# Kernel tuning notes

Measured on AMD Instinct MI355X. Metric: run time of the kernel, lower is better.

The kernel has to match this reference:

```python
import jax, jax.numpy as jnp
import numpy as np

B, L, H, P = 4, 8192, 256, 256


def discretize(log_real, imag, log_Delta, B_real, B_imag):
    # Lambda = -exp(log_real) + i*imag ; ZOH discretization
    Lr = -jnp.exp(log_real)
    Li = imag
    Delta = jnp.exp(log_Delta)
    ad = Lr * Delta
    bd = Li * Delta
    exp_ad = jnp.exp(ad)
    Lbar_r = exp_ad * jnp.cos(bd)
    Lbar_i = exp_ad * jnp.sin(bd)
    denom = jnp.maximum(Lr * Lr + Li * Li, 1e-12)
    inv_Lr = Lr / denom
    inv_Li = -Li / denom
    diff_r = Lbar_r - 1.0
    diff_i = Lbar_i
    coeff_r = inv_Lr * diff_r - inv_Li * diff_i
    coeff_i = inv_Lr * diff_i + inv_Li * diff_r
    B_bar_r = coeff_r[:, None] * B_real - coeff_i[:, None] * B_imag
    B_bar_i = coeff_r[:, None] * B_imag + coeff_i[:, None] * B_real
    return Lbar_r, Lbar_i, B_bar_r, B_bar_i


def binop(ei, ej):
    Ar_i, Ai_i, xr_i, xi_i = ei
    Ar_j, Ai_j, xr_j, xi_j = ej
    return (Ar_j * Ar_i - Ai_j * Ai_i,
            Ar_j * Ai_i + Ai_j * Ar_i,
            Ar_j * xr_i - Ai_j * xi_i + xr_j,
            Ar_j * xi_i + Ai_j * xr_i + xi_j)


def apply_ssm(Lbar_r, Lbar_i, B_bar_r, B_bar_i, C_real, C_imag, D, x):
    # x: (B,L,H), B_bar: (P,H), C: (H,P)
    Bu_r = jnp.einsum('blh,ph->blp', x, B_bar_r)
    Bu_i = jnp.einsum('blh,ph->blp', x, B_bar_i)
    A_r = jnp.broadcast_to(Lbar_r, Bu_r.shape)
    A_i = jnp.broadcast_to(Lbar_i, Bu_i.shape)
    _, _, xs_r, xs_i = jax.lax.associative_scan(binop, (A_r, A_i, Bu_r, Bu_i), axis=1)
    ys = jnp.einsum('blp,hp->blh', xs_r, C_real) - jnp.einsum('blp,hp->blh', xs_i, C_imag)
    return ys + D * x


def s5(log_real, imag, log_Delta, B_real, B_imag, C_real, C_imag, D, x):
    Lbar_r, Lbar_i, B_bar_r, B_bar_i = discretize(log_real, imag, log_Delta, B_real, B_imag)
    y = apply_ssm(Lbar_r, Lbar_i, B_bar_r, B_bar_i, C_real, C_imag, D, x)
    return jax.nn.gelu(y, approximate=False)


def setup_inputs() -> dict:
    key = jax.random.key(0)
    ks = jax.random.split(key, 17)
    std_b = 1.0 / H ** 0.5
    std_c = 1.0 / P ** 0.5
    def params(ki):
        k = jax.random.split(ks[ki], 8)
        return dict(
            log_real=jax.random.normal(k[0], (P,), jnp.float32) * 0.5,
            imag=jax.random.normal(k[1], (P,), jnp.float32),
            log_Delta=jnp.zeros((P,), jnp.float32),
            B_real=jax.random.normal(k[2], (P, H), jnp.float32) * std_b,
            B_imag=jax.random.normal(k[3], (P, H), jnp.float32) * std_b,
            C_real=jax.random.normal(k[4], (H, P), jnp.float32) * std_c,
            C_imag=jax.random.normal(k[5], (H, P), jnp.float32) * std_c,
            D=jnp.ones((H,), jnp.float32),
        )
    f = params(1)
    b = params(2)
    inp = {'x': jax.random.normal(ks[0], (B, L, H), jnp.float32)}
    for name, v in f.items():
        inp['fwd_' + name] = v
    for name, v in b.items():
        inp['bwd_' + name] = v
    return inp


def reference(x,
              fwd_log_real, fwd_imag, fwd_log_Delta, fwd_B_real, fwd_B_imag,
              fwd_C_real, fwd_C_imag, fwd_D,
              bwd_log_real, bwd_imag, bwd_log_Delta, bwd_B_real, bwd_B_imag,
              bwd_C_real, bwd_C_imag, bwd_D):
    x_flip = jnp.flip(x, axis=1)
    y_f = s5(fwd_log_real, fwd_imag, fwd_log_Delta, fwd_B_real, fwd_B_imag,
             fwd_C_real, fwd_C_imag, fwd_D, x)
    y_b = s5(bwd_log_real, bwd_imag, bwd_log_Delta, bwd_B_real, bwd_B_imag,
             bwd_C_real, bwd_C_imag, bwd_D, x_flip)
    return y_f + jnp.flip(y_b, axis=1)
```

## Files before the change

### kernel.cpp

```cpp
#include <hip/hip_runtime.h>
#include <math.h>

#define B_DIM 4
#define L_DIM 8192
#define H_DIM 256
#define P_DIM 256
#define M_DIM (B_DIM * L_DIM)
#define NC 64
#define LC 128

typedef __attribute__((ext_vector_type(8))) short bf16x8;
typedef __attribute__((ext_vector_type(4))) float f32x4;

static __device__ __forceinline__ float bf2f(unsigned int u) {
    union { unsigned int i; float f; } v; v.i = u << 16; return v.f;
}
static __device__ __forceinline__ unsigned short f2bf(float f) {
    union { float f; unsigned int i; } v; v.f = f;
    unsigned int r = v.i + 0x7FFFu + ((v.i >> 16) & 1u);
    return (unsigned short)(r >> 16);
}
static __device__ __forceinline__ float gelu_f(float x) {
    float z = 0.7978845608028654f * (x + 0.044715f * x * x * x);
    float e = __expf(2.0f * z);
    float t = 1.0f - 2.0f / (e + 1.0f);
    return 0.5f * x * (1.0f + t);
}
static __device__ __forceinline__ void async_load16(const void* g, void* l) {
    __builtin_amdgcn_global_load_lds(
        (const __attribute__((address_space(1))) unsigned int*)g,
        (__attribute__((address_space(3))) unsigned int*)l, 16, 0, 0);
}
static __device__ __forceinline__ float2 cmul2(float2 a, float2 b) {
    return make_float2(a.x * b.x - a.y * b.y, a.x * b.y + a.y * b.x);
}
static __device__ __forceinline__ float2 csq2(float2 a) {
    return make_float2(a.x * a.x - a.y * a.y, 2.f * a.x * a.y);
}
static __device__ __forceinline__ float2 cmad(float2 A, float2 s, float2 z) {
    return make_float2(A.x * s.x - A.y * s.y + z.x, A.x * s.y + A.y * s.x + z.y);
}

__global__ void prep_kernel(const float* fLr, const float* fIm, const float* fLd,
                            const float* fBr, const float* fBi,
                            const float* fCr, const float* fCi,
                            const float* bLr, const float* bIm, const float* bLd,
                            const float* bBr, const float* bBi,
                            const float* bCr, const float* bCi,
                            const float4* __restrict__ x4, ushort4* __restrict__ xb,
                            unsigned short* Bmat, unsigned short* B3, float2* LbarWS) {
    int gid = blockIdx.x * 256 + threadIdx.x;
    if (gid < 2097152) {
        float4 v = x4[gid];
        ushort4 o;
        o.x = f2bf(v.x); o.y = f2bf(v.y); o.z = f2bf(v.z); o.w = f2bf(v.w);
        xb[gid] = o;
        return;
    }
    int g1 = gid - 2097152;
    if (g1 < 262144) {
        int k = g1 >> 8, h = g1 & 255;
        int d = k >> 9, pc = k & 511, p = pc >> 1, comp = pc & 1;
        const float* LR = d ? bLr : fLr;
        const float* IM = d ? bIm : fIm;
        const float* LD = d ? bLd : fLd;
        const float* BR = d ? bBr : fBr;
        const float* BI = d ? bBi : fBi;
        float Lr = -expf(LR[p]);
        float Li = IM[p];
        float Delta = expf(LD[p]);
        float ea = expf(Lr * Delta);
        float bd = Li * Delta;
        float Lbr = ea * cosf(bd);
        float Lbi = ea * sinf(bd);
        float denom = fmaxf(Lr * Lr + Li * Li, 1e-12f);
        float ivr = Lr / denom, ivi = -Li / denom;
        float dr = Lbr - 1.0f, di = Lbi;
        float cr = ivr * dr - ivi * di;
        float ci = ivr * di + ivi * dr;
        float br = BR[p * 256 + h], bi = BI[p * 256 + h];
        float val = comp ? (cr * bi + ci * br) : (cr * br - ci * bi);
        Bmat[g1] = f2bf(val);
    } else if (g1 < 524288) {
        int g2 = g1 - 262144;
        int d = g2 >> 17;
        int rem = g2 & 131071;
        int h = rem >> 9;
        int kk = rem & 511;
        int p = kk >> 1, comp = kk & 1;
        const float* CR = d ? bCr : fCr;
        const float* CI = d ? bCi : fCi;
        float val = comp ? -CI[h * 256 + p] : CR[h * 256 + p];
        B3[g2] = f2bf(val);
    } else if (g1 < 524800) {
        int g2 = g1 - 524288;
        int d = g2 >> 8, p = g2 & 255;
        const float* LR = d ? bLr : fLr;
        const float* IM = d ? bIm : fIm;
        const float* LD = d ? bLd : fLd;
        float Lr = -expf(LR[p]); float Li = IM[p]; float Delta = expf(LD[p]);
        float ea = expf(Lr * Delta); float bd = Li * Delta;
        LbarWS[g2] = make_float2(ea * cosf(bd), ea * sinf(bd));
    }
}

__global__ __launch_bounds__(256, 2) void k1_gemm(const unsigned short* __restrict__ A,
                                                  const unsigned short* __restrict__ Bm,
                                                  unsigned short* __restrict__ Bu,
                                                  const float2* __restrict__ Lbar,
                                                  float2* __restrict__ carry,
                                                  float2* __restrict__ Usub) {
    __shared__ unsigned short SH[16384];
    __shared__ float2 Sbuf2[64][4];
    int tid = threadIdx.x;
    int lane = tid & 63, wv = tid >> 6;
    int wm = (wv >> 1) * 64, wn = (wv & 1) * 64;
    int Mb = blockIdx.x * 128, Nb = blockIdx.y * 128;
    int lr = lane >> 3;
    int swz = ((lane & 7) ^ lr) * 8;
    f32x4 acc[4][4];
#pragma unroll
    for (int i = 0; i < 4; i++)
#pragma unroll
        for (int j = 0; j < 4; j++) acc[i][j] = (f32x4){0.f, 0.f, 0.f, 0.f};
    int mrow = lane & 15, quad = lane >> 4;
    for (int kb = 0; kb < 256; kb += 64) {
#pragma unroll
        for (int ch = wv; ch < 16; ch += 4) {
            int r = ch * 8 + lr;
            async_load16(A  + (size_t)(Mb + r) * 256 + kb + swz, (char*)SH + ch * 1024);
            async_load16(Bm + (size_t)(Nb + r) * 256 + kb + swz, (char*)SH + 16384 + ch * 1024);
        }
        __syncthreads();
#pragma unroll
        for (int kk = 0; kk < 64; kk += 32) {
            bf16x8 af[4], bfr[4];
#pragma unroll
            for (int i = 0; i < 4; i++) {
                int rr = wm + 16 * i + mrow;
                af[i] = *(const bf16x8*)&SH[rr * 64 + ((((kk >> 3) + quad) ^ (rr & 7)) << 3)];
            }
#pragma unroll
            for (int j = 0; j < 4; j++) {
                int rr = wn + 16 * j + mrow;
                bfr[j] = *(const bf16x8*)&SH[8192 + rr * 64 + ((((kk >> 3) + quad) ^ (rr & 7)) << 3)];
            }
#pragma unroll
            for (int i = 0; i < 4; i++)
#pragma unroll
                for (int j = 0; j < 4; j++)
                    acc[i][j] = __builtin_amdgcn_mfma_f32_16x16x32_bf16(af[i], bfr[j], acc[i][j], 0, 0, 0);
        }
        __syncthreads();
    }
    unsigned short* Cs = SH;
#pragma unroll
    for (int i = 0; i < 4; i++)
#pragma unroll
        for (int j = 0; j < 4; j++)
#pragma unroll
            for (int r = 0; r < 4; r++) {
                int row = wm + 16 * i + quad * 4 + r;
                int col = wn + 16 * j + mrow;
                Cs[row * 128 + col] = f2bf(acc[i][j][r]);
            }
    __syncthreads();
#pragma unroll
    for (int it = 0; it < 8; it++) {
        int o = tid * 16 + it * 4096;
        int row = o >> 8, colb = o & 255;
        uint4 v = *(const uint4*)((const char*)Cs + o);
        *(uint4*)((char*)Bu + (size_t)(Mb + row) * 2048 + (size_t)Nb * 2 + colb) = v;
    }
    int d = Nb >> 9;
    int b = Mb >> 13;
    int c = (Mb >> 7) & 63;
    float2 s = make_float2(0.f, 0.f);
    float2 A2 = make_float2(0.f, 0.f);
    float2 snap[3];
    snap[0] = snap[1] = snap[2] = make_float2(0.f, 0.f);
    int p = 0;
    if (tid < 128) {
        int j = tid & 63, half = tid >> 6;
        p = ((Nb & 511) >> 1) + j;
        A2 = Lbar[d * 256 + p];
        const unsigned int* C32 = (const unsigned int*)Cs;
        int r0 = half * 64;
        if (d == 0) {
            for (int t = 0; t < 64; t++) {
                unsigned int v = C32[(r0 + t) * 64 + j];
                float2 z = make_float2(bf2f(v & 0xffffu), bf2f(v >> 16));
                s = cmad(A2, s, z);
                if ((t & 15) == 15 && t < 63) snap[t >> 4] = s;
            }
        } else {
            for (int t = 63; t >= 0; t--) {
                unsigned int v = C32[(r0 + t) * 64 + j];
                float2 z = make_float2(bf2f(v & 0xffffu), bf2f(v >> 16));
                s = cmad(A2, s, z);
                if ((t & 15) == 0 && t > 0) snap[(t >> 4) - 1] = s;
            }
        }
        if (half == 1) {
            Sbuf2[j][0] = snap[0]; Sbuf2[j][1] = snap[1];
            Sbuf2[j][2] = snap[2]; Sbuf2[j][3] = s;
        }
    }
    __syncthreads();
    if (tid < 64) {
        float2 h1a = Sbuf2[tid][0], h1b = Sbuf2[tid][1], h1c = Sbuf2[tid][2], S1 = Sbuf2[tid][3];
        float2 a16 = A2;
#pragma unroll
        for (int k = 0; k < 4; k++) a16 = csq2(a16);
        float2 a32 = csq2(a16);
        float2 a48 = cmul2(a32, a16);
        float2 a64 = csq2(a32);
        float2 S0 = s;
        float2 Uq[8];
        float2 cfull;
        float2 zero = make_float2(0.f, 0.f);
        if (d == 0) {
            Uq[0] = zero;  Uq[1] = snap[0]; Uq[2] = snap[1]; Uq[3] = snap[2];
            Uq[4] = S0;
            Uq[5] = cmad(a16, S0, h1a);
            Uq[6] = cmad(a32, S0, h1b);
            Uq[7] = cmad(a48, S0, h1c);
            cfull = cmad(a64, S0, S1);
        } else {
            Uq[7] = zero;
            Uq[6] = h1c;
            Uq[5] = h1b;
            Uq[4] = h1a;
            Uq[3] = S1;
            Uq[2] = cmad(a16, S1, snap[2]);
            Uq[1] = cmad(a32, S1, snap[1]);
            Uq[0] = cmad(a48, S1, snap[0]);
            cfull = cmad(a64, S1, S0);
        }
        size_t cidx = ((size_t)(d * 4 + b) * NC + c) * 256 + p;
        carry[cidx] = cfull;
        size_t ub = (((size_t)(d * 4 + b) * NC + c) * 8) * 256 + p;
#pragma unroll
        for (int q = 0; q < 8; q++) Usub[ub + (size_t)q * 256] = Uq[q];
    }
}

static __device__ __forceinline__ void k3_half(const unsigned short* __restrict__ XS,
                                               const unsigned short* __restrict__ B3h,
                                               unsigned short* As0, unsigned short* Bs0,
                                               unsigned short* As1, unsigned short* Bs1,
                                               const float2* Ptab, const float2* LbarL,
                                               const float2* __restrict__ Uchunk,
                                               int Mb, int Hb, int coff, int d,
                                               int wm, int wn, int mrow, int quad,
                                               int lr, int swz, int wv, int tid,
                                               f32x4 (&acc)[4][4]) {
    int j = tid & 31, q = tid >> 5;
    int r0 = q * 16;
    const float2* ubase = Uchunk + q * 256 + j;
#define STAGE_K3(KB, AB, BB)                                                                  \
    do {                                                                                      \
        _Pragma("unroll")                                                                     \
        for (int ch = wv; ch < 16; ch += 4) {                                                 \
            int r = ch * 8 + lr;                                                              \
            async_load16(XS + (size_t)(Mb + r) * 1024 + coff + (KB) + swz, (char*)(AB) + ch * 1024); \
            async_load16(B3h + (size_t)(Hb + r) * 512 + (KB) + swz, (char*)(BB) + ch * 1024); \
        }                                                                                     \
    } while (0)
    STAGE_K3(0, As0, Bs0);
    float2 Ucur = ubase[0];
    for (int st = 0; st < 8; st++) {
        int kb = st * 64;
        unsigned short* Ac = (st & 1) ? As1 : As0;
        unsigned short* Bc = (st & 1) ? Bs1 : Bs0;
        __syncthreads();
        float2 Unext = Ucur;
        if (st < 7) {
            STAGE_K3(kb + 64, (st & 1) ? As0 : As1, (st & 1) ? Bs0 : Bs1);
            Unext = ubase[(kb + 64) >> 1];
        }
        {
            int p = (kb >> 1) + j;
            float2 Ach = LbarL[d * 256 + p];
            float2 P  = Ptab[d * 256 + p];
            int e = d ? (7 - q) : q;
            float2 bp = Ach;
#pragma unroll
            for (int k = 0; k < 4; k++) bp = csq2(bp);
            float2 ap = make_float2(1.f, 0.f);
            if (e & 1) ap = cmul2(ap, bp);
            bp = csq2(bp);
            if (e & 2) ap = cmul2(ap, bp);
            bp = csq2(bp);
            if (e & 4) ap = cmul2(ap, bp);
            float2 sv = cmad(ap, P, Ucur);
            unsigned int* A32 = (unsigned int*)Ac;
            unsigned int zb[16];
#pragma unroll
            for (int tt = 0; tt < 16; tt++) {
                int row = r0 + tt;
                zb[tt] = A32[row * 32 + (((j >> 2) ^ (row & 7)) << 2) + (j & 3)];
            }
            if (d == 0) {
#pragma unroll
                for (int tt = 0; tt < 16; tt++) {
                    float2 z = make_float2(bf2f(zb[tt] & 0xffffu), bf2f(zb[tt] >> 16));
                    sv = cmad(Ach, sv, z);
                    zb[tt] = (unsigned int)f2bf(sv.x) | ((unsigned int)f2bf(sv.y) << 16);
                }
            } else {
#pragma unroll
                for (int tt = 15; tt >= 0; tt--) {
                    float2 z = make_float2(bf2f(zb[tt] & 0xffffu), bf2f(zb[tt] >> 16));
                    sv = cmad(Ach, sv, z);
                    zb[tt] = (unsigned int)f2bf(sv.x) | ((unsigned int)f2bf(sv.y) << 16);
                }
            }
#pragma unroll
            for (int tt = 0; tt < 16; tt++) {
                int row = r0 + tt;
                A32[row * 32 + (((j >> 2) ^ (row & 7)) << 2) + (j & 3)] = zb[tt];
            }
        }
        __syncthreads();
#pragma unroll
        for (int kk = 0; kk < 64; kk += 32) {
            bf16x8 af[4], bfr[4];
#pragma unroll
            for (int i = 0; i < 4; i++) {
                int rr = wm + 16 * i + mrow;
                af[i] = *(const bf16x8*)&Ac[rr * 64 + ((((kk >> 3) + quad) ^ (rr & 7)) << 3)];
            }
#pragma unroll
            for (int jj2 = 0; jj2 < 4; jj2++) {
                int rr = wn + 16 * jj2 + mrow;
                bfr[jj2] = *(const bf16x8*)&Bc[rr * 64 + ((((kk >> 3) + quad) ^ (rr & 7)) << 3)];
            }
#pragma unroll
            for (int i = 0; i < 4; i++)
#pragma unroll
                for (int jj2 = 0; jj2 < 4; jj2++)
                    acc[i][jj2] = __builtin_amdgcn_mfma_f32_16x16x32_bf16(af[i], bfr[jj2], acc[i][jj2], 0, 0, 0);
        }
        Ucur = Unext;
    }
#undef STAGE_K3
}

__global__ __launch_bounds__(256, 2) void k3_gemm(const unsigned short* __restrict__ XS,
                                                  const unsigned short* __restrict__ B3,
                                                  const unsigned short* __restrict__ xbf,
                                                  const float* __restrict__ Df,
                                                  const float* __restrict__ Db,
                                                  const float2* __restrict__ Lbar,
                                                  const float2* __restrict__ carry,
                                                  const float2* __restrict__ Usub,
                                                  float* __restrict__ out) {
    __shared__ unsigned short As0[8192], Bs0[8192];
    __shared__ unsigned short As1[8192], Bs1[8192];
    __shared__ float2 Ptab[512];
    __shared__ float2 LbarL[512];
    int tid = threadIdx.x;
    int lane = tid & 63, wv = tid >> 6;
    int wm = (wv >> 1) * 64, wn = (wv & 1) * 64;
    int Mb = blockIdx.x * 128, Hb = blockIdx.y * 128;
    int b = Mb >> 13, c = (Mb >> 7) & 63;
    int lr = lane >> 3;
    int swz = ((lane & 7) ^ lr) * 8;
    int mrow = lane & 15, quad = lane >> 4;
    {
        int p0 = tid;
#pragma unroll
        for (int d2 = 0; d2 < 2; d2++) {
            float2 A = Lbar[d2 * 256 + p0];
            LbarL[d2 * 256 + p0] = A;
            float2 a128 = A;
#pragma unroll
            for (int k = 0; k < 7; k++) a128 = csq2(a128);
            float2 s = make_float2(0.f, 0.f);
            const float2* cb = carry + ((size_t)(d2 * 4 + b) * NC) * 256 + p0;
            if (d2 == 0) {
#pragma unroll 16
                for (int jj = 0; jj < c; jj++) s = cmad(a128, s, cb[(size_t)jj * 256]);
            } else {
#pragma unroll 16
                for (int jj = NC - 1; jj > c; jj--) s = cmad(a128, s, cb[(size_t)jj * 256]);
            }
            Ptab[d2 * 256 + p0] = s;
        }
    }
    __syncthreads();
    f32x4 accf[4][4], accb[4][4];
#pragma unroll
    for (int i = 0; i < 4; i++)
#pragma unroll
        for (int j = 0; j < 4; j++) {
            accf[i][j] = (f32x4){0.f, 0.f, 0.f, 0.f};
            accb[i][j] = (f32x4){0.f, 0.f, 0.f, 0.f};
        }
    const float2* U0 = Usub + (((size_t)(0 * 4 + b) * NC + c) * 8) * 256;
    const float2* U1 = Usub + (((size_t)(1 * 4 + b) * NC + c) * 8) * 256;
    k3_half(XS, B3,          As0, Bs0, As1, Bs1, Ptab, LbarL, U0, Mb, Hb, 0,   0,
            wm, wn, mrow, quad, lr, swz, wv, tid, accf);
    k3_half(XS, B3 + 131072, As0, Bs0, As1, Bs1, Ptab, LbarL, U1, Mb, Hb, 512, 1,
            wm, wn, mrow, quad, lr, swz, wv, tid, accb);
#pragma unroll
    for (int i = 0; i < 4; i++)
#pragma unroll
        for (int j = 0; j < 4; j++) {
            int h = Hb + wn + 16 * j + mrow;
            float df = Df[h], db = Db[h];
#pragma unroll
            for (int r = 0; r < 4; r++) {
                int row = Mb + wm + 16 * i + quad * 4 + r;
                float xv = bf2f((unsigned int)xbf[(size_t)row * 256 + h]);
                float yf = accf[i][j][r] + df * xv;
                float yb = accb[i][j][r] + db * xv;
                out[(size_t)row * 256 + h] = gelu_f(yf) + gelu_f(yb);
            }
        }
}

extern "C" void kernel_launch(void* const* d_in, const int* in_sizes, int n_in,
                              void* d_out, int out_size, void* d_ws, size_t ws_size,
                              hipStream_t stream) {
    const float* x   = (const float*)d_in[0];
    const float* fLr = (const float*)d_in[1];
    const float* fIm = (const float*)d_in[2];
    const float* fLd = (const float*)d_in[3];
    const float* fBr = (const float*)d_in[4];
    const float* fBi = (const float*)d_in[5];
    const float* fCr = (const float*)d_in[6];
    const float* fCi = (const float*)d_in[7];
    const float* fD  = (const float*)d_in[8];
    const float* bLr = (const float*)d_in[9];
    const float* bIm = (const float*)d_in[10];
    const float* bLd = (const float*)d_in[11];
    const float* bBr = (const float*)d_in[12];
    const float* bBi = (const float*)d_in[13];
    const float* bCr = (const float*)d_in[14];
    const float* bCi = (const float*)d_in[15];
    const float* bD  = (const float*)d_in[16];
    float* out = (float*)d_out;

    char* ws = (char*)d_ws;
    unsigned short* xbf  = (unsigned short*)(ws);
    unsigned short* Bu   = (unsigned short*)(ws + 16777216);
    unsigned short* Bmat = (unsigned short*)(ws + 16777216 + 67108864);
    unsigned short* B3   = (unsigned short*)(ws + 16777216 + 67108864 + 524288);
    float2* LbarWS = (float2*)(ws + 16777216 + 67108864 + 1048576);
    float2* carry  = (float2*)(ws + 16777216 + 67108864 + 1048576 + 4096);
    float2* Usub   = (float2*)(ws + 16777216 + 67108864 + 1048576 + 4096 + 1048576);

    prep_kernel<<<10242, 256, 0, stream>>>(fLr, fIm, fLd, fBr, fBi, fCr, fCi,
                                           bLr, bIm, bLd, bBr, bBi, bCr, bCi,
                                           (const float4*)x, (ushort4*)xbf,
                                           Bmat, B3, LbarWS);
    k1_gemm<<<dim3(256, 8), 256, 0, stream>>>(xbf, Bmat, Bu, LbarWS, carry, Usub);
    k3_gemm<<<dim3(256, 2), 256, 0, stream>>>(Bu, B3, xbf, fD, bD, LbarWS, carry, Usub, out);
}
```

Baseline: 193.2 us.

## Shrink k3 tile to 128x64, single-buffer LDS, raise occupancy

The k3 GEMM kernel now uses a 128x64 output tile instead of 128x128 and launches twice as many blocks. It drops the double-buffered LDS staging for a single buffer and merges the forward and backward halves into one 16-step loop. Smaller accumulators and LDS footprint allow launch_bounds of 3 blocks per CU, trading software pipelining for occupancy. The risks are that each block redoes the in-LDS chunk scan for its A tile, and the carry/Ptab prefix computation is duplicated across twice as many blocks.

```diff
diff --git a/kernel.cpp b/kernel.cpp
--- a/kernel.cpp
+++ b/kernel.cpp
@@ -245,109 +245,7 @@
     }
 }
 
-static __device__ __forceinline__ void k3_half(const unsigned short* __restrict__ XS,
-                                               const unsigned short* __restrict__ B3h,
-                                               unsigned short* As0, unsigned short* Bs0,
-                                               unsigned short* As1, unsigned short* Bs1,
-                                               const float2* Ptab, const float2* LbarL,
-                                               const float2* __restrict__ Uchunk,
-                                               int Mb, int Hb, int coff, int d,
-                                               int wm, int wn, int mrow, int quad,
-                                               int lr, int swz, int wv, int tid,
-                                               f32x4 (&acc)[4][4]) {
-    int j = tid & 31, q = tid >> 5;
-    int r0 = q * 16;
-    const float2* ubase = Uchunk + q * 256 + j;
-#define STAGE_K3(KB, AB, BB)                                                                  \
-    do {                                                                                      \
-        _Pragma("unroll")                                                                     \
-        for (int ch = wv; ch < 16; ch += 4) {                                                 \
-            int r = ch * 8 + lr;                                                              \
-            async_load16(XS + (size_t)(Mb + r) * 1024 + coff + (KB) + swz, (char*)(AB) + ch * 1024); \
-            async_load16(B3h + (size_t)(Hb + r) * 512 + (KB) + swz, (char*)(BB) + ch * 1024); \
-        }                                                                                     \
-    } while (0)
-    STAGE_K3(0, As0, Bs0);
-    float2 Ucur = ubase[0];
-    for (int st = 0; st < 8; st++) {
-        int kb = st * 64;
-        unsigned short* Ac = (st & 1) ? As1 : As0;
-        unsigned short* Bc = (st & 1) ? Bs1 : Bs0;
-        __syncthreads();
-        float2 Unext = Ucur;
-        if (st < 7) {
-            STAGE_K3(kb + 64, (st & 1) ? As0 : As1, (st & 1) ? Bs0 : Bs1);
-            Unext = ubase[(kb + 64) >> 1];
-        }
-        {
-            int p = (kb >> 1) + j;
-            float2 Ach = LbarL[d * 256 + p];
-            float2 P  = Ptab[d * 256 + p];
-            int e = d ? (7 - q) : q;
-            float2 bp = Ach;
-#pragma unroll
-            for (int k = 0; k < 4; k++) bp = csq2(bp);
-            float2 ap = make_float2(1.f, 0.f);
-            if (e & 1) ap = cmul2(ap, bp);
-            bp = csq2(bp);
-            if (e & 2) ap = cmul2(ap, bp);
-            bp = csq2(bp);
-            if (e & 4) ap = cmul2(ap, bp);
-            float2 sv = cmad(ap, P, Ucur);
-            unsigned int* A32 = (unsigned int*)Ac;
-            unsigned int zb[16];
-#pragma unroll
-            for (int tt = 0; tt < 16; tt++) {
-                int row = r0 + tt;
-                zb[tt] = A32[row * 32 + (((j >> 2) ^ (row & 7)) << 2) + (j & 3)];
-            }
-            if (d == 0) {
-#pragma unroll
-                for (int tt = 0; tt < 16; tt++) {
-                    float2 z = make_float2(bf2f(zb[tt] & 0xffffu), bf2f(zb[tt] >> 16));
-                    sv = cmad(Ach, sv, z);
-                    zb[tt] = (unsigned int)f2bf(sv.x) | ((unsigned int)f2bf(sv.y) << 16);
-                }
-            } else {
-#pragma unroll
-                for (int tt = 15; tt >= 0; tt--) {
-                    float2 z = make_float2(bf2f(zb[tt] & 0xffffu), bf2f(zb[tt] >> 16));
-                    sv = cmad(Ach, sv, z);
-                    zb[tt] = (unsigned int)f2bf(sv.x) | ((unsigned int)f2bf(sv.y) << 16);
-                }
-            }
-#pragma unroll
-            for (int tt = 0; tt < 16; tt++) {
-                int row = r0 + tt;
-                A32[row * 32 + (((j >> 2) ^ (row & 7)) << 2) + (j & 3)] = zb[tt];
-            }
-        }
-        __syncthreads();
-#pragma unroll
-        for (int kk = 0; kk < 64; kk += 32) {
-            bf16x8 af[4], bfr[4];
-#pragma unroll
-            for (int i = 0; i < 4; i++) {
-                int rr = wm + 16 * i + mrow;
-                af[i] = *(const bf16x8*)&Ac[rr * 64 + ((((kk >> 3) + quad) ^ (rr & 7)) << 3)];
-            }
-#pragma unroll
-            for (int jj2 = 0; jj2 < 4; jj2++) {
-                int rr = wn + 16 * jj2 + mrow;
-                bfr[jj2] = *(const bf16x8*)&Bc[rr * 64 + ((((kk >> 3) + quad) ^ (rr & 7)) << 3)];
-            }
-#pragma unroll
-            for (int i = 0; i < 4; i++)
-#pragma unroll
-                for (int jj2 = 0; jj2 < 4; jj2++)
-                    acc[i][jj2] = __builtin_amdgcn_mfma_f32_16x16x32_bf16(af[i], bfr[jj2], acc[i][jj2], 0, 0, 0);
-        }
-        Ucur = Unext;
-    }
-#undef STAGE_K3
-}
-
-__global__ __launch_bounds__(256, 2) void k3_gemm(const unsigned short* __restrict__ XS,
+__global__ __launch_bounds__(256, 3) void k3_gemm(const unsigned short* __restrict__ XS,
                                                   const unsigned short* __restrict__ B3,
                                                   const unsigned short* __restrict__ xbf,
                                                   const float* __restrict__ Df,
@@ -356,25 +254,27 @@
                                                   const float2* __restrict__ carry,
                                                   const float2* __restrict__ Usub,
                                                   float* __restrict__ out) {
-    __shared__ unsigned short As0[8192], Bs0[8192];
-    __shared__ unsigned short As1[8192], Bs1[8192];
+    __shared__ unsigned short As[8192];
+    __shared__ unsigned short Bs[4096];
     __shared__ float2 Ptab[512];
     __shared__ float2 LbarL[512];
     int tid = threadIdx.x;
     int lane = tid & 63, wv = tid >> 6;
-    int wm = (wv >> 1) * 64, wn = (wv & 1) * 64;
-    int Mb = blockIdx.x * 128, Hb = blockIdx.y * 128;
+    int Mb = blockIdx.x * 128, Hb = blockIdx.y * 64;
     int b = Mb >> 13, c = (Mb >> 7) & 63;
     int lr = lane >> 3;
     int swz = ((lane & 7) ^ lr) * 8;
     int mrow = lane & 15, quad = lane >> 4;
+    int j = tid & 31, q = tid >> 5;
+    int r0 = q * 16;
+
     {
         int p0 = tid;
 #pragma unroll
         for (int d2 = 0; d2 < 2; d2++) {
-            float2 A = Lbar[d2 * 256 + p0];
-            LbarL[d2 * 256 + p0] = A;
-            float2 a128 = A;
+            float2 Av = Lbar[d2 * 256 + p0];
+            LbarL[d2 * 256 + p0] = Av;
+            float2 a128 = Av;
 #pragma unroll
             for (int k = 0; k < 7; k++) a128 = csq2(a128);
             float2 s = make_float2(0.f, 0.f);
@@ -389,33 +289,121 @@
             Ptab[d2 * 256 + p0] = s;
         }
     }
-    __syncthreads();
-    f32x4 accf[4][4], accb[4][4];
-#pragma unroll
-    for (int i = 0; i < 4; i++)
-#pragma unroll
-        for (int j = 0; j < 4; j++) {
-            accf[i][j] = (f32x4){0.f, 0.f, 0.f, 0.f};
-            accb[i][j] = (f32x4){0.f, 0.f, 0.f, 0.f};
-        }
-    const float2* U0 = Usub + (((size_t)(0 * 4 + b) * NC + c) * 8) * 256;
-    const float2* U1 = Usub + (((size_t)(1 * 4 + b) * NC + c) * 8) * 256;
-    k3_half(XS, B3,          As0, Bs0, As1, Bs1, Ptab, LbarL, U0, Mb, Hb, 0,   0,
-            wm, wn, mrow, quad, lr, swz, wv, tid, accf);
-    k3_half(XS, B3 + 131072, As0, Bs0, As1, Bs1, Ptab, LbarL, U1, Mb, Hb, 512, 1,
-            wm, wn, mrow, quad, lr, swz, wv, tid, accb);
-#pragma unroll
-    for (int i = 0; i < 4; i++)
-#pragma unroll
-        for (int j = 0; j < 4; j++) {
-            int h = Hb + wn + 16 * j + mrow;
+
+    f32x4 accf[2][4], accb[2][4];
+#pragma unroll
+    for (int i = 0; i < 2; i++)
+#pragma unroll
+        for (int jj = 0; jj < 4; jj++) {
+            accf[i][jj] = (f32x4){0.f, 0.f, 0.f, 0.f};
+            accb[i][jj] = (f32x4){0.f, 0.f, 0.f, 0.f};
+        }
+
+    const float2* Ub0 = Usub + (((size_t)(0 * 4 + b) * NC + c) * 8 + q) * 256 + j;
+    const float2* Ub1 = Usub + (((size_t)(1 * 4 + b) * NC + c) * 8 + q) * 256 + j;
+
+    for (int t = 0; t < 16; ++t) {
+        int d2 = t >> 3;
+        int kb = (t & 7) * 64;
+        const unsigned short* B3h = B3 + d2 * 131072;
+#pragma unroll
+        for (int ch = wv; ch < 16; ch += 4) {
+            int r = ch * 8 + lr;
+            async_load16(XS + (size_t)(Mb + r) * 1024 + t * 64 + swz, (char*)As + ch * 1024);
+        }
+#pragma unroll
+        for (int ch = wv; ch < 8; ch += 4) {
+            int r = ch * 8 + lr;
+            async_load16(B3h + (size_t)(Hb + r) * 512 + kb + swz, (char*)Bs + ch * 1024);
+        }
+        float2 Uc = (d2 ? Ub1 : Ub0)[(size_t)(t & 7) * 32];
+        __syncthreads();
+        {
+            int p = (t & 7) * 32 + j;
+            float2 Ach = LbarL[d2 * 256 + p];
+            float2 P = Ptab[d2 * 256 + p];
+            int e = d2 ? (7 - q) : q;
+            float2 bp = Ach;
+#pragma unroll
+            for (int k = 0; k < 4; k++) bp = csq2(bp);
+            float2 ap = make_float2(1.f, 0.f);
+            if (e & 1) ap = cmul2(ap, bp);
+            bp = csq2(bp);
+            if (e & 2) ap = cmul2(ap, bp);
+            bp = csq2(bp);
+            if (e & 4) ap = cmul2(ap, bp);
+            float2 sv = cmad(ap, P, Uc);
+            unsigned int* A32 = (unsigned int*)As;
+            unsigned int zb[16];
+#pragma unroll
+            for (int tt = 0; tt < 16; tt++) {
+                int row = r0 + tt;
+                zb[tt] = A32[row * 32 + (((j >> 2) ^ (row & 7)) << 2) + (j & 3)];
+            }
+            if (d2 == 0) {
+#pragma unroll
+                for (int tt = 0; tt < 16; tt++) {
+                    float2 z = make_float2(bf2f(zb[tt] & 0xffffu), bf2f(zb[tt] >> 16));
+                    sv = cmad(Ach, sv, z);
+                    zb[tt] = (unsigned int)f2bf(sv.x) | ((unsigned int)f2bf(sv.y) << 16);
+                }
+            } else {
+#pragma unroll
+                for (int tt = 15; tt >= 0; tt--) {
+                    float2 z = make_float2(bf2f(zb[tt] & 0xffffu), bf2f(zb[tt] >> 16));
+                    sv = cmad(Ach, sv, z);
+                    zb[tt] = (unsigned int)f2bf(sv.x) | ((unsigned int)f2bf(sv.y) << 16);
+                }
+            }
+#pragma unroll
+            for (int tt = 0; tt < 16; tt++) {
+                int row = r0 + tt;
+                A32[row * 32 + (((j >> 2) ^ (row & 7)) << 2) + (j & 3)] = zb[tt];
+            }
+        }
+        __syncthreads();
+#pragma unroll
+        for (int kk = 0; kk < 64; kk += 32) {
+            bf16x8 af[2], bfr[4];
+#pragma unroll
+            for (int i = 0; i < 2; i++) {
+                int rr = wv * 32 + 16 * i + mrow;
+                af[i] = *(const bf16x8*)&As[rr * 64 + ((((kk >> 3) + quad) ^ (rr & 7)) << 3)];
+            }
+#pragma unroll
+            for (int jj = 0; jj < 4; jj++) {
+                int rr = 16 * jj + mrow;
+                bfr[jj] = *(const bf16x8*)&Bs[rr * 64 + ((((kk >> 3) + quad) ^ (rr & 7)) << 3)];
+            }
+            if (t < 8) {
+#pragma unroll
+                for (int i = 0; i < 2; i++)
+#pragma unroll
+                    for (int jj = 0; jj < 4; jj++)
+                        accf[i][jj] = __builtin_amdgcn_mfma_f32_16x16x32_bf16(af[i], bfr[jj], accf[i][jj], 0, 0, 0);
+            } else {
+#pragma unroll
+                for (int i = 0; i < 2; i++)
+#pragma unroll
+                    for (int jj = 0; jj < 4; jj++)
+                        accb[i][jj] = __builtin_amdgcn_mfma_f32_16x16x32_bf16(af[i], bfr[jj], accb[i][jj], 0, 0, 0);
+            }
+        }
+        __syncthreads();
+    }
+
+#pragma unroll
+    for (int i = 0; i < 2; i++)
+#pragma unroll
+        for (int jj = 0; jj < 4; jj++) {
+            int h = Hb + 16 * jj + mrow;
             float df = Df[h], db = Db[h];
 #pragma unroll
             for (int r = 0; r < 4; r++) {
-                int row = Mb + wm + 16 * i + quad * 4 + r;
+                int row = Mb + wv * 32 + 16 * i + quad * 4 + r;
                 float xv = bf2f((unsigned int)xbf[(size_t)row * 256 + h]);
-                float yf = accf[i][j][r] + df * xv;
-                float yb = accb[i][j][r] + db * xv;
+                float yf = accf[i][jj][r] + df * xv;
+                float yb = accb[i][jj][r] + db * xv;
                 out[(size_t)row * 256 + h] = gelu_f(yf) + gelu_f(yb);
             }
         }
@@ -457,5 +445,5 @@
                                            (const float4*)x, (ushort4*)xbf,
                                            Bmat, B3, LbarWS);
     k1_gemm<<<dim3(256, 8), 256, 0, stream>>>(xbf, Bmat, Bu, LbarWS, carry, Usub);
-    k3_gemm<<<dim3(256, 2), 256, 0, stream>>>(Bu, B3, xbf, fD, bD, LbarWS, carry, Usub, out);
-}
+    k3_gemm<<<dim3(256, 4), 256, 0, stream>>>(Bu, B3, xbf, fD, bD, LbarWS, carry, Usub, out);
+}
```

Result: slower. 235.8 us (+22.1%).

## Single-buffer k3 LDS tiles, precompute Lbar^16 table, cheaper bf16 unpack

Applied to the files above, without the earlier changes.

Replaces the double-buffered A/B LDS staging in the k3 GEMM with a single buffer: each k-step loads, syncs, runs the in-LDS scan, runs the MFMAs, then syncs again. This halves the tile LDS footprint, likely so that more blocks can be resident per CU, at the cost of no longer overlapping the next tile's global loads with compute. It also precomputes Lbar^16 once per block into shared memory instead of repeating four complex squarings each step, and unpacks bf16 pairs with shift/mask bit operations.

```diff
diff --git a/kernel.cpp b/kernel.cpp
--- a/kernel.cpp
+++ b/kernel.cpp
@@ -15,10 +15,16 @@
 static __device__ __forceinline__ float bf2f(unsigned int u) {
     union { unsigned int i; float f; } v; v.i = u << 16; return v.f;
 }
+static __device__ __forceinline__ float bits2f(unsigned int u) {
+    union { unsigned int i; float f; } v; v.i = u; return v.f;
+}
 static __device__ __forceinline__ unsigned short f2bf(float f) {
     union { float f; unsigned int i; } v; v.f = f;
     unsigned int r = v.i + 0x7FFFu + ((v.i >> 16) & 1u);
     return (unsigned short)(r >> 16);
+}
+static __device__ __forceinline__ unsigned int pack_bf16i(float x, float y) {
+    return (unsigned int)f2bf(x) | ((unsigned int)f2bf(y) << 16);
 }
 static __device__ __forceinline__ float gelu_f(float x) {
     float z = 0.7978845608028654f * (x + 0.044715f * x * x * x);
@@ -247,9 +253,9 @@
 
 static __device__ __forceinline__ void k3_half(const unsigned short* __restrict__ XS,
                                                const unsigned short* __restrict__ B3h,
-                                               unsigned short* As0, unsigned short* Bs0,
-                                               unsigned short* As1, unsigned short* Bs1,
+                                               unsigned short* As, unsigned short* Bs,
                                                const float2* Ptab, const float2* LbarL,
+                                               const float2* La16L,
                                                const float2* __restrict__ Uchunk,
                                                int Mb, int Hb, int coff, int d,
                                                int wm, int wn, int mrow, int quad,
@@ -258,35 +264,22 @@
     int j = tid & 31, q = tid >> 5;
     int r0 = q * 16;
     const float2* ubase = Uchunk + q * 256 + j;
-#define STAGE_K3(KB, AB, BB)                                                                  \
-    do {                                                                                      \
-        _Pragma("unroll")                                                                     \
-        for (int ch = wv; ch < 16; ch += 4) {                                                 \
-            int r = ch * 8 + lr;                                                              \
-            async_load16(XS + (size_t)(Mb + r) * 1024 + coff + (KB) + swz, (char*)(AB) + ch * 1024); \
-            async_load16(B3h + (size_t)(Hb + r) * 512 + (KB) + swz, (char*)(BB) + ch * 1024); \
-        }                                                                                     \
-    } while (0)
-    STAGE_K3(0, As0, Bs0);
-    float2 Ucur = ubase[0];
     for (int st = 0; st < 8; st++) {
         int kb = st * 64;
-        unsigned short* Ac = (st & 1) ? As1 : As0;
-        unsigned short* Bc = (st & 1) ? Bs1 : Bs0;
+#pragma unroll
+        for (int ch = wv; ch < 16; ch += 4) {
+            int r = ch * 8 + lr;
+            async_load16(XS + (size_t)(Mb + r) * 1024 + coff + kb + swz, (char*)As + ch * 1024);
+            async_load16(B3h + (size_t)(Hb + r) * 512 + kb + swz, (char*)Bs + ch * 1024);
+        }
+        float2 Ucur = ubase[kb >> 1];
         __syncthreads();
-        float2 Unext = Ucur;
-        if (st < 7) {
-            STAGE_K3(kb + 64, (st & 1) ? As0 : As1, (st & 1) ? Bs0 : Bs1);
-            Unext = ubase[(kb + 64) >> 1];
-        }
         {
             int p = (kb >> 1) + j;
             float2 Ach = LbarL[d * 256 + p];
             float2 P  = Ptab[d * 256 + p];
             int e = d ? (7 - q) : q;
-            float2 bp = Ach;
-#pragma unroll
-            for (int k = 0; k < 4; k++) bp = csq2(bp);
+            float2 bp = La16L[d * 256 + p];
             float2 ap = make_float2(1.f, 0.f);
             if (e & 1) ap = cmul2(ap, bp);
             bp = csq2(bp);
@@ -294,7 +287,7 @@
             bp = csq2(bp);
             if (e & 4) ap = cmul2(ap, bp);
             float2 sv = cmad(ap, P, Ucur);
-            unsigned int* A32 = (unsigned int*)Ac;
+            unsigned int* A32 = (unsigned int*)As;
             unsigned int zb[16];
 #pragma unroll
             for (int tt = 0; tt < 16; tt++) {
@@ -304,16 +297,16 @@
             if (d == 0) {
 #pragma unroll
                 for (int tt = 0; tt < 16; tt++) {
-                    float2 z = make_float2(bf2f(zb[tt] & 0xffffu), bf2f(zb[tt] >> 16));
+                    float2 z = make_float2(bits2f(zb[tt] << 16), bits2f(zb[tt] & 0xffff0000u));
                     sv = cmad(Ach, sv, z);
-                    zb[tt] = (unsigned int)f2bf(sv.x) | ((unsigned int)f2bf(sv.y) << 16);
+                    zb[tt] = pack_bf16i(sv.x, sv.y);
                 }
             } else {
 #pragma unroll
                 for (int tt = 15; tt >= 0; tt--) {
-                    float2 z = make_float2(bf2f(zb[tt] & 0xffffu), bf2f(zb[tt] >> 16));
+                    float2 z = make_float2(bits2f(zb[tt] << 16), bits2f(zb[tt] & 0xffff0000u));
                     sv = cmad(Ach, sv, z);
-                    zb[tt] = (unsigned int)f2bf(sv.x) | ((unsigned int)f2bf(sv.y) << 16);
+                    zb[tt] = pack_bf16i(sv.x, sv.y);
                 }
             }
 #pragma unroll
@@ -329,12 +322,12 @@
 #pragma unroll
             for (int i = 0; i < 4; i++) {
                 int rr = wm + 16 * i + mrow;
-                af[i] = *(const bf16x8*)&Ac[rr * 64 + ((((kk >> 3) + quad) ^ (rr & 7)) << 3)];
+                af[i] = *(const bf16x8*)&As[rr * 64 + ((((kk >> 3) + quad) ^ (rr & 7)) << 3)];
             }
 #pragma unroll
             for (int jj2 = 0; jj2 < 4; jj2++) {
                 int rr = wn + 16 * jj2 + mrow;
-                bfr[jj2] = *(const bf16x8*)&Bc[rr * 64 + ((((kk >> 3) + quad) ^ (rr & 7)) << 3)];
+                bfr[jj2] = *(const bf16x8*)&Bs[rr * 64 + ((((kk >> 3) + quad) ^ (rr & 7)) << 3)];
             }
 #pragma unroll
             for (int i = 0; i < 4; i++)
@@ -342,9 +335,8 @@
                 for (int jj2 = 0; jj2 < 4; jj2++)
                     acc[i][jj2] = __builtin_amdgcn_mfma_f32_16x16x32_bf16(af[i], bfr[jj2], acc[i][jj2], 0, 0, 0);
         }
-        Ucur = Unext;
-    }
-#undef STAGE_K3
+        __syncthreads();
+    }
 }
 
 __global__ __launch_bounds__(256, 2) void k3_gemm(const unsigned short* __restrict__ XS,
@@ -356,10 +348,10 @@
                                                   const float2* __restrict__ carry,
                                                   const float2* __restrict__ Usub,
                                                   float* __restrict__ out) {
-    __shared__ unsigned short As0[8192], Bs0[8192];
-    __shared__ unsigned short As1[8192], Bs1[8192];
+    __shared__ unsigned short As[8192], Bs[8192];
     __shared__ float2 Ptab[512];
     __shared__ float2 LbarL[512];
+    __shared__ float2 La16L[512];
     int tid = threadIdx.x;
     int lane = tid & 63, wv = tid >> 6;
     int wm = (wv >> 1) * 64, wn = (wv & 1) * 64;
@@ -374,9 +366,13 @@
         for (int d2 = 0; d2 < 2; d2++) {
             float2 A = Lbar[d2 * 256 + p0];
             LbarL[d2 * 256 + p0] = A;
-            float2 a128 = A;
-#pragma unroll
-            for (int k = 0; k < 7; k++) a128 = csq2(a128);
+            float2 apow = A;
+#pragma unroll
+            for (int k = 0; k < 4; k++) apow = csq2(apow);
+            La16L[d2 * 256 + p0] = apow;
+#pragma unroll
+            for (int k = 0; k < 3; k++) apow = csq2(apow);
+            float2 a128 = apow;
             float2 s = make_float2(0.f, 0.f);
             const float2* cb = carry + ((size_t)(d2 * 4 + b) * NC) * 256 + p0;
             if (d2 == 0) {
@@ -400,9 +396,9 @@
         }
     const float2* U0 = Usub + (((size_t)(0 * 4 + b) * NC + c) * 8) * 256;
     const float2* U1 = Usub + (((size_t)(1 * 4 + b) * NC + c) * 8) * 256;
-    k3_half(XS, B3,          As0, Bs0, As1, Bs1, Ptab, LbarL, U0, Mb, Hb, 0,   0,
+    k3_half(XS, B3,          As, Bs, Ptab, LbarL, La16L, U0, Mb, Hb, 0,   0,
             wm, wn, mrow, quad, lr, swz, wv, tid, accf);
-    k3_half(XS, B3 + 131072, As0, Bs0, As1, Bs1, Ptab, LbarL, U1, Mb, Hb, 512, 1,
+    k3_half(XS, B3 + 131072, As, Bs, Ptab, LbarL, La16L, U1, Mb, Hb, 512, 1,
             wm, wn, mrow, quad, lr, swz, wv, tid, accb);
 #pragma unroll
     for (int i = 0; i < 4; i++)
```

Result: slower. 197.4 us (+2.2%).
